# Kernel optimization log

Hardware: AMD Instinct MI355X
Metric: run time of the kernel (lower is better)

Reference implementation:

```python
import jax, jax.numpy as jnp
import numpy as np

EPS = 1e-5
N, F, D = 16384, 1024, 8


def setup_inputs() -> dict:
    key = jax.random.key(0)
    k1, k2, k3, k4 = jax.random.split(key, 4)
    x = jax.random.normal(k1, (N, F), dtype=jnp.float32)
    y = jax.random.randint(k2, (N,), 0, D, dtype=jnp.int64)
    # per-domain affine params (BatchNorm1d weight/bias per domain)
    gamma = 1.0 + 0.1 * jax.random.normal(k3, (D, F), dtype=jnp.float32)
    beta = 0.1 * jax.random.normal(k4, (D, F), dtype=jnp.float32)
    return {"x": x, "y": y, "gamma": gamma, "beta": beta}


def reference(x, y, gamma, beta):
    # Domain-specific batchnorm (training mode): per-domain batch stats,
    # biased variance, affine. Domains with 1 sample pass through x;
    # domains with 0 samples contribute nothing (out stays zero).
    d = gamma.shape[0]
    ones = jnp.ones((x.shape[0],), dtype=x.dtype)
    counts = jax.ops.segment_sum(ones, y, num_segments=d)          # [D]
    s1 = jax.ops.segment_sum(x, y, num_segments=d)                 # [D, F]
    s2 = jax.ops.segment_sum(x * x, y, num_segments=d)             # [D, F]
    cnt = jnp.maximum(counts, 1.0)[:, None]                        # avoid /0
    mean = s1 / cnt                                                # [D, F]
    var = s2 / cnt - mean * mean                                   # biased var
    inv = jax.lax.rsqrt(var + EPS)                                 # [D, F]
    xhat = (x - mean[y]) * inv[y]                                  # [N, F]
    out_bn = gamma[y] * xhat + beta[y]
    c = counts[y][:, None]                                         # [N, 1]
    return jnp.where(c > 1.0, out_bn, jnp.where(c == 1.0, x, jnp.zeros_like(x)))
```

## Files before the change

### kernel.cpp

```cpp
#include <hip/hip_runtime.h>


#define EPSV 1e-5f
constexpr int N = 16384;
constexpr int F = 1024;
constexpr int D = 8;
constexpr int ROWS_PER_BLOCK = 64;
constexpr int RG = N / ROWS_PER_BLOCK;

__global__ __launch_bounds__(256) void k1_partials(
    const float* __restrict__ x, const int* __restrict__ y,
    float* __restrict__ partials, int* __restrict__ cnt_parts) {
  const int t = threadIdx.x;
  const int rg = blockIdx.x >> 1;
  const int h = blockIdx.x & 1;

  __shared__ int hist[D];
  if (t < D) hist[t] = 0;
  __syncthreads();
  if (h == 0 && t < ROWS_PER_BLOCK) {
    int d = y[rg * ROWS_PER_BLOCK + t];
    atomicAdd(&hist[d], 1);
  }
  __syncthreads();
  if (h == 0 && t < D) cnt_parts[rg * D + t] = hist[t];

  float2 a1[D], a2[D];
#pragma unroll
  for (int k = 0; k < D; ++k) {
    a1[k] = make_float2(0.f, 0.f);
    a2[k] = make_float2(0.f, 0.f);
  }

  const float2* __restrict__ x2 = (const float2*)x;
  const int col2 = h * 256 + t;
  const int row0 = rg * ROWS_PER_BLOCK;

#define ACC(K)                            \
  a1[K].x += v.x;                         \
  a1[K].y += v.y;                         \
  a2[K].x = fmaf(v.x, v.x, a2[K].x);      \
  a2[K].y = fmaf(v.y, v.y, a2[K].y);      \
  break;

  for (int r = 0; r < ROWS_PER_BLOCK; r += 8) {
    const int n = row0 + r;
    int dd[8];
    float2 vv[8];
#pragma unroll
    for (int j = 0; j < 8; ++j) dd[j] = y[n + j];
#pragma unroll
    for (int j = 0; j < 8; ++j) vv[j] = x2[(n + j) * 512 + col2];
#pragma unroll
    for (int j = 0; j < 8; ++j) {
      float2 v = vv[j];
      switch (dd[j]) {
        case 0: ACC(0)
        case 1: ACC(1)
        case 2: ACC(2)
        case 3: ACC(3)
        case 4: ACC(4)
        case 5: ACC(5)
        case 6: ACC(6)
        case 7: ACC(7)
      }
    }
  }
#undef ACC

  float4* __restrict__ p4 = (float4*)partials;
#pragma unroll
  for (int k = 0; k < D; ++k) {
    float4 w = make_float4(a1[k].x, a2[k].x, a1[k].y, a2[k].y);
    p4[(rg * D + k) * 512 + h * 256 + t] = w;
  }
}

__global__ __launch_bounds__(256) void k2_stats(
    const float* __restrict__ partials, const int* __restrict__ cnt_parts,
    const float* __restrict__ gamma, const float* __restrict__ beta,
    float* __restrict__ scale, float* __restrict__ shift) {
  const int t = threadIdx.x;
  const int i = t & 31;
  const int ch = t >> 5;
  const int p = blockIdx.x * 32 + i;
  const int d = p >> 10;

  __shared__ int sc[256];
  sc[t] = cnt_parts[t * D + d];

  const float2* __restrict__ pp = (const float2*)partials;
  float s1 = 0.f, s2 = 0.f;
#pragma unroll 8
  for (int r = 0; r < 32; ++r) {
    const int rg = ch * 32 + r;
    float2 v = pp[(size_t)rg * (D * F) + p];
    s1 += v.x;
    s2 += v.y;
  }

  __shared__ float sf[8][32][2];
  sf[ch][i][0] = s1;
  sf[ch][i][1] = s2;
  __syncthreads();
  for (int s = 128; s > 0; s >>= 1) {
    if (t < s) sc[t] += sc[t + s];
    __syncthreads();
  }

  if (t < 32) {
    float r1 = 0.f, r2 = 0.f;
#pragma unroll
    for (int c = 0; c < 8; ++c) {
      r1 += sf[c][t][0];
      r2 += sf[c][t][1];
    }
    const int pw = blockIdx.x * 32 + t;
    const float c = (float)sc[0];
    const float cc = fmaxf(c, 1.f);
    const float mean = r1 / cc;
    const float var = r2 / cc - mean * mean;
    const float inv = rsqrtf(var + EPSV);
    float scv = gamma[pw] * inv;
    float shv = beta[pw] - mean * scv;
    if (c <= 1.f) {
      scv = (c == 1.f) ? 1.f : 0.f;
      shv = 0.f;
    }
    scale[pw] = scv;
    shift[pw] = shv;
  }
}

__global__ __launch_bounds__(256) void k3_apply(
    const float* __restrict__ x, const int* __restrict__ y,
    const float* __restrict__ scale, const float* __restrict__ shift,
    float* __restrict__ out) {
  const int t = threadIdx.x;
  const int n0 = blockIdx.x * 8;

  int dd[8];
#pragma unroll
  for (int j = 0; j < 8; ++j) dd[j] = y[n0 + j];

#pragma unroll
  for (int j = 0; j < 8; ++j) {
    const int n = n0 + j;
    const float4 v = ((const float4*)x)[n * 256 + t];
    const float4 g = ((const float4*)scale)[dd[j] * 256 + t];
    const float4 b = ((const float4*)shift)[dd[j] * 256 + t];
    float4 o;
    o.x = fmaf(v.x, g.x, b.x);
    o.y = fmaf(v.y, g.y, b.y);
    o.z = fmaf(v.z, g.z, b.z);
    o.w = fmaf(v.w, g.w, b.w);
    ((float4*)out)[n * 256 + t] = o;
  }
}

extern "C" void kernel_launch(void* const* d_in, const int* in_sizes, int n_in,
                              void* d_out, int out_size, void* d_ws, size_t ws_size,
                              hipStream_t stream) {
  const float* x = (const float*)d_in[0];
  const int* y = (const int*)d_in[1];
  const float* gamma = (const float*)d_in[2];
  const float* beta = (const float*)d_in[3];
  float* out = (float*)d_out;

  float* partials = (float*)d_ws;
  int* cnt_parts = (int*)(partials + (size_t)RG * D * F * 2);
  float* scale = (float*)(cnt_parts + RG * D);
  float* shift = scale + D * F;

  k1_partials<<<RG * 2, 256, 0, stream>>>(x, y, partials, cnt_parts);
  k2_stats<<<256, 256, 0, stream>>>(partials, cnt_parts, gamma, beta, scale, shift);
  k3_apply<<<N / 8, 256, 0, stream>>>(x, y, scale, shift, out);
}
```

Measured before the change: 135.9 us.

## Fuse stats, reduction and apply into one cooperative kernel with grid syncs

Replaces the three kernels with one cooperative kernel of 256 blocks of 512 threads. Each block accumulates per-domain partial sums over its 64 rows with software-prefetched loads, then grid-syncs, reduces partials into scale and shift, grid-syncs again, and applies the affine transform to the same rows using nontemporal stores. This removes two launch gaps and aims to re-read its x rows from cache. In exchange it pays two grid-wide barriers and runs on only 256 blocks, which limits memory-level parallelism on a large GPU.

Measured after the change: 215.9 us. +58.8%, slower.

```diff
diff --git a/kernel.cpp b/kernel.cpp
--- a/kernel.cpp
+++ b/kernel.cpp
@@ -1,29 +1,37 @@
 #include <hip/hip_runtime.h>
+#include <hip/hip_cooperative_groups.h>
+
+namespace cg = cooperative_groups;
 
 
 #define EPSV 1e-5f
 constexpr int N = 16384;
 constexpr int F = 1024;
 constexpr int D = 8;
-constexpr int ROWS_PER_BLOCK = 64;
-constexpr int RG = N / ROWS_PER_BLOCK;
-
-__global__ __launch_bounds__(256) void k1_partials(
+constexpr int NB = 256;
+constexpr int NT = 512;
+constexpr int RPB = N / NB;
+constexpr int F2 = F / 2;
+
+typedef float f32x2 __attribute__((ext_vector_type(2)));
+
+__global__ __launch_bounds__(NT, 2) void fused_dsbn(
     const float* __restrict__ x, const int* __restrict__ y,
-    float* __restrict__ partials, int* __restrict__ cnt_parts) {
+    const float* __restrict__ gamma, const float* __restrict__ beta,
+    float* __restrict__ out, float* __restrict__ partials,
+    int* __restrict__ cnt_parts, float* __restrict__ scale,
+    float* __restrict__ shift) {
   const int t = threadIdx.x;
-  const int rg = blockIdx.x >> 1;
-  const int h = blockIdx.x & 1;
+  const int b = blockIdx.x;
+  const int row0 = b * RPB;
 
   __shared__ int hist[D];
+  __shared__ int sc[NB];
+  __shared__ float sf[16][32][2];
+
   if (t < D) hist[t] = 0;
   __syncthreads();
-  if (h == 0 && t < ROWS_PER_BLOCK) {
-    int d = y[rg * ROWS_PER_BLOCK + t];
-    atomicAdd(&hist[d], 1);
-  }
-  __syncthreads();
-  if (h == 0 && t < D) cnt_parts[rg * D + t] = hist[t];
+  if (t < RPB) atomicAdd(&hist[y[row0 + t]], 1);
 
   float2 a1[D], a2[D];
 #pragma unroll
@@ -33,24 +41,32 @@
   }
 
   const float2* __restrict__ x2 = (const float2*)x;
-  const int col2 = h * 256 + t;
-  const int row0 = rg * ROWS_PER_BLOCK;
-
-#define ACC(K)                            \
-  a1[K].x += v.x;                         \
-  a1[K].y += v.y;                         \
-  a2[K].x = fmaf(v.x, v.x, a2[K].x);      \
-  a2[K].y = fmaf(v.y, v.y, a2[K].y);      \
+
+#define ACC(K)                         \
+  a1[K].x += v.x;                      \
+  a1[K].y += v.y;                      \
+  a2[K].x = fmaf(v.x, v.x, a2[K].x);   \
+  a2[K].y = fmaf(v.y, v.y, a2[K].y);   \
   break;
 
-  for (int r = 0; r < ROWS_PER_BLOCK; r += 8) {
-    const int n = row0 + r;
-    int dd[8];
-    float2 vv[8];
-#pragma unroll
-    for (int j = 0; j < 8; ++j) dd[j] = y[n + j];
-#pragma unroll
-    for (int j = 0; j < 8; ++j) vv[j] = x2[(n + j) * 512 + col2];
+  float2 vv[8];
+  int dd[8];
+#pragma unroll
+  for (int j = 0; j < 8; ++j) {
+    dd[j] = y[row0 + j];
+    vv[j] = x2[(size_t)(row0 + j) * F2 + t];
+  }
+#pragma unroll
+  for (int r = 0; r < RPB; r += 8) {
+    float2 nv[8];
+    int nd[8];
+    if (r + 8 < RPB) {
+#pragma unroll
+      for (int j = 0; j < 8; ++j) {
+        nd[j] = y[row0 + r + 8 + j];
+        nv[j] = x2[(size_t)(row0 + r + 8 + j) * F2 + t];
+      }
+    }
 #pragma unroll
     for (int j = 0; j < 8; ++j) {
       float2 v = vv[j];
@@ -65,96 +81,102 @@
         case 7: ACC(7)
       }
     }
+    if (r + 8 < RPB) {
+#pragma unroll
+      for (int j = 0; j < 8; ++j) {
+        vv[j] = nv[j];
+        dd[j] = nd[j];
+      }
+    }
   }
 #undef ACC
 
   float4* __restrict__ p4 = (float4*)partials;
 #pragma unroll
-  for (int k = 0; k < D; ++k) {
-    float4 w = make_float4(a1[k].x, a2[k].x, a1[k].y, a2[k].y);
-    p4[(rg * D + k) * 512 + h * 256 + t] = w;
-  }
-}
-
-__global__ __launch_bounds__(256) void k2_stats(
-    const float* __restrict__ partials, const int* __restrict__ cnt_parts,
-    const float* __restrict__ gamma, const float* __restrict__ beta,
-    float* __restrict__ scale, float* __restrict__ shift) {
-  const int t = threadIdx.x;
-  const int i = t & 31;
-  const int ch = t >> 5;
-  const int p = blockIdx.x * 32 + i;
-  const int d = p >> 10;
-
-  __shared__ int sc[256];
-  sc[t] = cnt_parts[t * D + d];
-
-  const float2* __restrict__ pp = (const float2*)partials;
-  float s1 = 0.f, s2 = 0.f;
-#pragma unroll 8
-  for (int r = 0; r < 32; ++r) {
-    const int rg = ch * 32 + r;
-    float2 v = pp[(size_t)rg * (D * F) + p];
-    s1 += v.x;
-    s2 += v.y;
-  }
-
-  __shared__ float sf[8][32][2];
-  sf[ch][i][0] = s1;
-  sf[ch][i][1] = s2;
+  for (int k = 0; k < D; ++k)
+    p4[(size_t)(b * D + k) * F2 + t] =
+        make_float4(a1[k].x, a2[k].x, a1[k].y, a2[k].y);
+
   __syncthreads();
-  for (int s = 128; s > 0; s >>= 1) {
-    if (t < s) sc[t] += sc[t + s];
+  if (t < D) cnt_parts[b * D + t] = hist[t];
+
+  cg::this_grid().sync();
+
+  {
+    const int i = t & 31;
+    const int ch = t >> 5;
+    const int p = b * 32 + i;
+    const int d = b >> 5;
+    const int f = p & (F - 1);
+
+    if (t < NB) sc[t] = cnt_parts[t * D + d];
+
+    const float2* __restrict__ pf2 = (const float2*)partials;
+    float s1 = 0.f, s2 = 0.f;
+#pragma unroll
+    for (int r = 0; r < 16; ++r) {
+      const int rg = ch * 16 + r;
+      float2 v = pf2[(size_t)(rg * D + d) * F + f];
+      s1 += v.x;
+      s2 += v.y;
+    }
+    sf[ch][i][0] = s1;
+    sf[ch][i][1] = s2;
     __syncthreads();
-  }
-
-  if (t < 32) {
-    float r1 = 0.f, r2 = 0.f;
-#pragma unroll
-    for (int c = 0; c < 8; ++c) {
-      r1 += sf[c][t][0];
-      r2 += sf[c][t][1];
-    }
-    const int pw = blockIdx.x * 32 + t;
-    const float c = (float)sc[0];
-    const float cc = fmaxf(c, 1.f);
-    const float mean = r1 / cc;
-    const float var = r2 / cc - mean * mean;
-    const float inv = rsqrtf(var + EPSV);
-    float scv = gamma[pw] * inv;
-    float shv = beta[pw] - mean * scv;
-    if (c <= 1.f) {
-      scv = (c == 1.f) ? 1.f : 0.f;
-      shv = 0.f;
-    }
-    scale[pw] = scv;
-    shift[pw] = shv;
-  }
-}
-
-__global__ __launch_bounds__(256) void k3_apply(
-    const float* __restrict__ x, const int* __restrict__ y,
-    const float* __restrict__ scale, const float* __restrict__ shift,
-    float* __restrict__ out) {
-  const int t = threadIdx.x;
-  const int n0 = blockIdx.x * 8;
-
-  int dd[8];
-#pragma unroll
-  for (int j = 0; j < 8; ++j) dd[j] = y[n0 + j];
-
-#pragma unroll
-  for (int j = 0; j < 8; ++j) {
-    const int n = n0 + j;
-    const float4 v = ((const float4*)x)[n * 256 + t];
-    const float4 g = ((const float4*)scale)[dd[j] * 256 + t];
-    const float4 b = ((const float4*)shift)[dd[j] * 256 + t];
-    float4 o;
-    o.x = fmaf(v.x, g.x, b.x);
-    o.y = fmaf(v.y, g.y, b.y);
-    o.z = fmaf(v.z, g.z, b.z);
-    o.w = fmaf(v.w, g.w, b.w);
-    ((float4*)out)[n * 256 + t] = o;
+    for (int s = 128; s > 0; s >>= 1) {
+      if (t < s) sc[t] += sc[t + s];
+      __syncthreads();
+    }
+
+    if (t < 32) {
+      float r1 = 0.f, r2 = 0.f;
+#pragma unroll
+      for (int c = 0; c < 16; ++c) {
+        r1 += sf[c][t][0];
+        r2 += sf[c][t][1];
+      }
+      const int pw = b * 32 + t;
+      const float c = (float)sc[0];
+      const float cc = fmaxf(c, 1.f);
+      const float mean = r1 / cc;
+      const float var = r2 / cc - mean * mean;
+      const float inv = rsqrtf(var + EPSV);
+      float scv = gamma[pw] * inv;
+      float shv = beta[pw] - mean * scv;
+      if (c <= 1.f) {
+        scv = (c == 1.f) ? 1.f : 0.f;
+        shv = 0.f;
+      }
+      scale[pw] = scv;
+      shift[pw] = shv;
+    }
+  }
+
+  cg::this_grid().sync();
+
+  {
+    const float2* __restrict__ g2 = (const float2*)scale;
+    const float2* __restrict__ h2 = (const float2*)shift;
+    f32x2* __restrict__ o2 = (f32x2*)out;
+#pragma unroll
+    for (int r = 0; r < RPB; r += 8) {
+      int dd2[8];
+      float2 xv[8];
+#pragma unroll
+      for (int j = 0; j < 8; ++j) dd2[j] = y[row0 + r + j];
+#pragma unroll
+      for (int j = 0; j < 8; ++j)
+        xv[j] = x2[(size_t)(row0 + r + j) * F2 + t];
+#pragma unroll
+      for (int j = 0; j < 8; ++j) {
+        const float2 g = g2[dd2[j] * F2 + t];
+        const float2 s = h2[dd2[j] * F2 + t];
+        f32x2 o;
+        o.x = fmaf(xv[j].x, g.x, s.x);
+        o.y = fmaf(xv[j].y, g.y, s.y);
+        __builtin_nontemporal_store(o, &o2[(size_t)(row0 + r + j) * F2 + t]);
+      }
+    }
   }
 }
 
@@ -168,11 +190,13 @@
   float* out = (float*)d_out;
 
   float* partials = (float*)d_ws;
-  int* cnt_parts = (int*)(partials + (size_t)RG * D * F * 2);
-  float* scale = (float*)(cnt_parts + RG * D);
+  int* cnt_parts = (int*)(partials + (size_t)NB * D * F * 2);
+  float* scale = (float*)(cnt_parts + NB * D);
   float* shift = scale + D * F;
 
-  k1_partials<<<RG * 2, 256, 0, stream>>>(x, y, partials, cnt_parts);
-  k2_stats<<<256, 256, 0, stream>>>(partials, cnt_parts, gamma, beta, scale, shift);
-  k3_apply<<<N / 8, 256, 0, stream>>>(x, y, scale, shift, out);
+  void* args[] = {(void*)&x,        (void*)&y,         (void*)&gamma,
+                  (void*)&beta,     (void*)&out,       (void*)&partials,
+                  (void*)&cnt_parts, (void*)&scale,    (void*)&shift};
+  hipLaunchCooperativeKernel((const void*)fused_dsbn, dim3(NB), dim3(NT), args,
+                             0, stream);
 }
```

## Halve rows per partial block, software-pipeline loads, widen stats grid, nontemporal output stores

Applied to the files above, without the earlier changes.

The partial-sum kernel now handles 32 rows per block, which doubles the grid, and prefetches the next 8 rows' x and y values while accumulating the current ones. The stats kernel runs 1024 blocks, each reducing 8 columns over the now 512 row groups. The apply kernel issues all x loads up front and writes the output with nontemporal stores. The goal is more memory parallelism and better latency hiding, at the cost of twice the partial-sum workspace traffic and more register pressure.

Result: slower. 147.7 us (+8.6%).

```diff
diff --git a/kernel.cpp b/kernel.cpp
--- a/kernel.cpp
+++ b/kernel.cpp
@@ -5,8 +5,11 @@
 constexpr int N = 16384;
 constexpr int F = 1024;
 constexpr int D = 8;
-constexpr int ROWS_PER_BLOCK = 64;
-constexpr int RG = N / ROWS_PER_BLOCK;
+constexpr int RPB = 32;
+constexpr int RG = N / RPB;
+constexpr int F2 = F / 2;
+
+typedef float f32x4 __attribute__((ext_vector_type(4)));
 
 __global__ __launch_bounds__(256) void k1_partials(
     const float* __restrict__ x, const int* __restrict__ y,
@@ -14,16 +17,12 @@
   const int t = threadIdx.x;
   const int rg = blockIdx.x >> 1;
   const int h = blockIdx.x & 1;
+  const int row0 = rg * RPB;
 
   __shared__ int hist[D];
   if (t < D) hist[t] = 0;
   __syncthreads();
-  if (h == 0 && t < ROWS_PER_BLOCK) {
-    int d = y[rg * ROWS_PER_BLOCK + t];
-    atomicAdd(&hist[d], 1);
-  }
-  __syncthreads();
-  if (h == 0 && t < D) cnt_parts[rg * D + t] = hist[t];
+  if (h == 0 && t < RPB) atomicAdd(&hist[y[row0 + t]], 1);
 
   float2 a1[D], a2[D];
 #pragma unroll
@@ -33,24 +32,33 @@
   }
 
   const float2* __restrict__ x2 = (const float2*)x;
-  const int col2 = h * 256 + t;
-  const int row0 = rg * ROWS_PER_BLOCK;
+  const int c = h * 256 + t;
 
-#define ACC(K)                            \
-  a1[K].x += v.x;                         \
-  a1[K].y += v.y;                         \
-  a2[K].x = fmaf(v.x, v.x, a2[K].x);      \
-  a2[K].y = fmaf(v.y, v.y, a2[K].y);      \
+#define ACC(K)                         \
+  a1[K].x += v.x;                      \
+  a1[K].y += v.y;                      \
+  a2[K].x = fmaf(v.x, v.x, a2[K].x);   \
+  a2[K].y = fmaf(v.y, v.y, a2[K].y);   \
   break;
 
-  for (int r = 0; r < ROWS_PER_BLOCK; r += 8) {
-    const int n = row0 + r;
-    int dd[8];
-    float2 vv[8];
+  float2 vv[8];
+  int dd[8];
 #pragma unroll
-    for (int j = 0; j < 8; ++j) dd[j] = y[n + j];
+  for (int j = 0; j < 8; ++j) {
+    dd[j] = y[row0 + j];
+    vv[j] = x2[(size_t)(row0 + j) * F2 + c];
+  }
 #pragma unroll
-    for (int j = 0; j < 8; ++j) vv[j] = x2[(n + j) * 512 + col2];
+  for (int r = 0; r < RPB; r += 8) {
+    float2 nv[8];
+    int nd[8];
+    if (r + 8 < RPB) {
+#pragma unroll
+      for (int j = 0; j < 8; ++j) {
+        nd[j] = y[row0 + r + 8 + j];
+        nv[j] = x2[(size_t)(row0 + r + 8 + j) * F2 + c];
+      }
+    }
 #pragma unroll
     for (int j = 0; j < 8; ++j) {
       float2 v = vv[j];
@@ -65,15 +73,24 @@
         case 7: ACC(7)
       }
     }
+    if (r + 8 < RPB) {
+#pragma unroll
+      for (int j = 0; j < 8; ++j) {
+        vv[j] = nv[j];
+        dd[j] = nd[j];
+      }
+    }
   }
 #undef ACC
 
   float4* __restrict__ p4 = (float4*)partials;
 #pragma unroll
-  for (int k = 0; k < D; ++k) {
-    float4 w = make_float4(a1[k].x, a2[k].x, a1[k].y, a2[k].y);
-    p4[(rg * D + k) * 512 + h * 256 + t] = w;
-  }
+  for (int k = 0; k < D; ++k)
+    p4[(size_t)(rg * D + k) * F2 + c] =
+        make_float4(a1[k].x, a2[k].x, a1[k].y, a2[k].y);
+
+  __syncthreads();
+  if (h == 0 && t < D) cnt_parts[rg * D + t] = hist[t];
 }
 
 __global__ __launch_bounds__(256) void k2_stats(
@@ -81,25 +98,25 @@
     const float* __restrict__ gamma, const float* __restrict__ beta,
     float* __restrict__ scale, float* __restrict__ shift) {
   const int t = threadIdx.x;
-  const int i = t & 31;
-  const int ch = t >> 5;
-  const int p = blockIdx.x * 32 + i;
+  const int i = t & 7;
+  const int ch = t >> 3;
+  const int p = blockIdx.x * 8 + i;
   const int d = p >> 10;
 
   __shared__ int sc[256];
-  sc[t] = cnt_parts[t * D + d];
+  sc[t] = cnt_parts[t * D + d] + cnt_parts[(t + 256) * D + d];
 
   const float2* __restrict__ pp = (const float2*)partials;
   float s1 = 0.f, s2 = 0.f;
-#pragma unroll 8
-  for (int r = 0; r < 32; ++r) {
-    const int rg = ch * 32 + r;
+#pragma unroll
+  for (int r = 0; r < 16; ++r) {
+    const int rg = ch * 16 + r;
     float2 v = pp[(size_t)rg * (D * F) + p];
     s1 += v.x;
     s2 += v.y;
   }
 
-  __shared__ float sf[8][32][2];
+  __shared__ float sf[32][8][2];
   sf[ch][i][0] = s1;
   sf[ch][i][1] = s2;
   __syncthreads();
@@ -108,14 +125,14 @@
     __syncthreads();
   }
 
-  if (t < 32) {
+  if (t < 8) {
     float r1 = 0.f, r2 = 0.f;
 #pragma unroll
-    for (int c = 0; c < 8; ++c) {
+    for (int c = 0; c < 32; ++c) {
       r1 += sf[c][t][0];
       r2 += sf[c][t][1];
     }
-    const int pw = blockIdx.x * 32 + t;
+    const int pw = blockIdx.x * 8 + t;
     const float c = (float)sc[0];
     const float cc = fmaxf(c, 1.f);
     const float mean = r1 / cc;
@@ -143,18 +160,22 @@
 #pragma unroll
   for (int j = 0; j < 8; ++j) dd[j] = y[n0 + j];
 
+  float4 xv[8];
+#pragma unroll
+  for (int j = 0; j < 8; ++j)
+    xv[j] = ((const float4*)x)[(size_t)(n0 + j) * 256 + t];
+
+  f32x4* __restrict__ o4 = (f32x4*)out;
 #pragma unroll
   for (int j = 0; j < 8; ++j) {
-    const int n = n0 + j;
-    const float4 v = ((const float4*)x)[n * 256 + t];
     const float4 g = ((const float4*)scale)[dd[j] * 256 + t];
     const float4 b = ((const float4*)shift)[dd[j] * 256 + t];
-    float4 o;
-    o.x = fmaf(v.x, g.x, b.x);
-    o.y = fmaf(v.y, g.y, b.y);
-    o.z = fmaf(v.z, g.z, b.z);
-    o.w = fmaf(v.w, g.w, b.w);
-    ((float4*)out)[n * 256 + t] = o;
+    f32x4 o;
+    o.x = fmaf(xv[j].x, g.x, b.x);
+    o.y = fmaf(xv[j].y, g.y, b.y);
+    o.z = fmaf(xv[j].z, g.z, b.z);
+    o.w = fmaf(xv[j].w, g.w, b.w);
+    __builtin_nontemporal_store(o, &o4[(size_t)(n0 + j) * 256 + t]);
   }
 }
 
@@ -173,6 +194,6 @@
   float* shift = scale + D * F;
 
   k1_partials<<<RG * 2, 256, 0, stream>>>(x, y, partials, cnt_parts);
-  k2_stats<<<256, 256, 0, stream>>>(partials, cnt_parts, gamma, beta, scale, shift);
+  k2_stats<<<1024, 256, 0, stream>>>(partials, cnt_parts, gamma, beta, scale, shift);
   k3_apply<<<N / 8, 256, 0, stream>>>(x, y, scale, shift, out);
 }
```
